# Kernel tuning notes

Hardware: AMD Instinct MI355X
Metric: run time of the kernel (lower is better)

## Reference

```python
import jax, jax.numpy as jnp
import numpy as np

INPUT_SIZE = 128
HIDDEN_SIZE = 128
BATCH = 65536
K = INPUT_SIZE + HIDDEN_SIZE


def setup_inputs() -> dict:
    key = jax.random.key(0)
    ks = jax.random.split(key, 11)
    bound = 1.0 / np.sqrt(K)  # nn.Linear default init range
    inp = {
        "input": jax.random.normal(ks[0], (BATCH, INPUT_SIZE), dtype=jnp.float32),
        "hidden": jax.random.normal(ks[1], (BATCH, HIDDEN_SIZE), dtype=jnp.float32),
        "cell": jax.random.normal(ks[2], (BATCH, HIDDEN_SIZE), dtype=jnp.float32),
        # Four gate linears: weights [hidden, K], biases [hidden]
        "W_f": jax.random.uniform(ks[3], (HIDDEN_SIZE, K), jnp.float32, -bound, bound),
        "b_f": jax.random.uniform(ks[4], (HIDDEN_SIZE,), jnp.float32, -bound, bound),
        "W_i": jax.random.uniform(ks[5], (HIDDEN_SIZE, K), jnp.float32, -bound, bound),
        "b_i": jax.random.uniform(ks[6], (HIDDEN_SIZE,), jnp.float32, -bound, bound),
        "W_o": jax.random.uniform(ks[7], (HIDDEN_SIZE, K), jnp.float32, -bound, bound),
        "b_o": jax.random.uniform(ks[8], (HIDDEN_SIZE,), jnp.float32, -bound, bound),
        "W_c": jax.random.uniform(ks[9], (HIDDEN_SIZE, K), jnp.float32, -bound, bound),
        "b_c": jax.random.uniform(ks[10], (HIDDEN_SIZE,), jnp.float32, -bound, bound),
    }
    return inp


def reference(input, hidden, cell, W_f, b_f, W_i, b_i, W_o, b_o, W_c, b_c):
    # combined = cat([input, hidden], axis=1); fuse 4 gate GEMMs into one
    combined = jnp.concatenate([input, hidden], axis=1)  # [B, K]
    W = jnp.concatenate([W_f, W_i, W_o, W_c], axis=0)    # [4H, K]
    b = jnp.concatenate([b_f, b_i, b_o, b_c], axis=0)    # [4H]
    gates = combined @ W.T + b                            # [B, 4H]
    f, i, o, g = jnp.split(gates, 4, axis=1)
    forget_gate = jax.nn.sigmoid(f)
    input_gate = jax.nn.sigmoid(i)
    output_gate = jax.nn.sigmoid(o)
    cell_gate = jnp.tanh(g)
    new_cell = forget_gate * cell + input_gate * cell_gate
    new_hidden = output_gate * jnp.tanh(new_cell)
    return (new_hidden, new_cell)
```

## Files before the change

kernel.cpp:

```cpp
#include <hip/hip_runtime.h>
#include <hip/hip_bf16.h>

#define BATCH   65536
#define FEAT    128
#define KDIM    256

typedef __attribute__((ext_vector_type(8))) short bf16x8;
typedef __attribute__((ext_vector_type(4))) float f32x4;

__device__ __forceinline__ short f2bf(float f) {
    return __builtin_bit_cast(short, __float2bfloat16(f));
}

__device__ __forceinline__ bf16x8 cvt8(f32x4 lo, f32x4 hi) {
    bf16x8 r;
    r[0] = f2bf(lo[0]); r[1] = f2bf(lo[1]); r[2] = f2bf(lo[2]); r[3] = f2bf(lo[3]);
    r[4] = f2bf(hi[0]); r[5] = f2bf(hi[1]); r[6] = f2bf(hi[2]); r[7] = f2bf(hi[3]);
    return r;
}

__device__ __forceinline__ float sigmoidf_(float x) {
    return 1.0f / (1.0f + __expf(-x));
}
__device__ __forceinline__ float tanhf_(float x) {
    float xc = fminf(fmaxf(x, -15.0f), 15.0f);
    float e = __expf(-2.0f * xc);
    return (1.0f - e) / (1.0f + e);
}

__global__ __launch_bounds__(256, 2)
void lstm_fused(const float* __restrict__ inp, const float* __restrict__ hid,
                const float* __restrict__ cel,
                const float* __restrict__ Wf, const float* __restrict__ bf_,
                const float* __restrict__ Wi, const float* __restrict__ bi_,
                const float* __restrict__ Wo, const float* __restrict__ bo_,
                const float* __restrict__ Wc, const float* __restrict__ bc_,
                float* __restrict__ out)
{
    const int tid  = threadIdx.x;
    const int lane = tid & 63;
    const int wid  = tid >> 6;
    const int b    = blockIdx.x;
    const int u      = b >> 3;
    const int xcd    = b & 7;
    const int rtBase = xcd * 32 + (u >> 1);
    const int cg     = ((u & 1) << 2) | wid;

    const int lr = lane & 15;
    const int lk = lane >> 4;
    const int j  = cg * 16 + lr;

    bf16x8 w[4][8];
    {
        const float* wsrc[4] = {Wf, Wi, Wo, Wc};
        #pragma unroll
        for (int g = 0; g < 4; ++g) {
            const float* src = wsrc[g] + (size_t)j * KDIM + lk * 8;
            #pragma unroll
            for (int ks = 0; ks < 8; ++ks) {
                f32x4 lo = *(const f32x4*)(src + ks * 32);
                f32x4 hi = *(const f32x4*)(src + ks * 32 + 4);
                w[g][ks] = cvt8(lo, hi);
            }
        }
    }
    const float bsf = bf_[j], bsi = bi_[j], bso = bo_[j], bsc = bc_[j];

    float* outH = out;
    float* outC = out + (size_t)BATCH * FEAT;

    for (int it = 0; it < 8; ++it) {
        const int R0 = (rtBase + it * 256) * 32;

        const float* aInp = inp + (size_t)(R0 + lr) * FEAT + lk * 8;
        const float* aHid = hid + (size_t)(R0 + lr) * FEAT + lk * 8;

        float cv[8];
        #pragma unroll
        for (int mb = 0; mb < 2; ++mb)
            #pragma unroll
            for (int t = 0; t < 4; ++t)
                cv[mb * 4 + t] = cel[(size_t)(R0 + mb * 16 + lk * 4 + t) * FEAT + j];

        f32x4 acc[2][4];
        #pragma unroll
        for (int mb = 0; mb < 2; ++mb)
            #pragma unroll
            for (int t = 0; t < 4; ++t) {
                acc[mb][0][t] = bsf; acc[mb][1][t] = bsi;
                acc[mb][2][t] = bso; acc[mb][3][t] = bsc;
            }

        f32x4 plo[2][2], phi[2][2];
        #pragma unroll
        for (int mb = 0; mb < 2; ++mb) {
            plo[0][mb] = *(const f32x4*)(aInp + mb * 16 * FEAT);
            phi[0][mb] = *(const f32x4*)(aInp + mb * 16 * FEAT + 4);
        }

        #pragma unroll
        for (int ks = 0; ks < 8; ++ks) {
            const int cur = ks & 1, nxt = cur ^ 1;
            if (ks < 7) {
                const float* nb2 = ((ks + 1) < 4 ? aInp : aHid) + ((ks + 1) & 3) * 32;
                #pragma unroll
                for (int mb = 0; mb < 2; ++mb) {
                    plo[nxt][mb] = *(const f32x4*)(nb2 + mb * 16 * FEAT);
                    phi[nxt][mb] = *(const f32x4*)(nb2 + mb * 16 * FEAT + 4);
                }
            }
            bf16x8 a0 = cvt8(plo[cur][0], phi[cur][0]);
            bf16x8 a1 = cvt8(plo[cur][1], phi[cur][1]);
            #pragma unroll
            for (int g = 0; g < 4; ++g) {
                acc[0][g] = __builtin_amdgcn_mfma_f32_16x16x32_bf16(a0, w[g][ks], acc[0][g], 0, 0, 0);
                acc[1][g] = __builtin_amdgcn_mfma_f32_16x16x32_bf16(a1, w[g][ks], acc[1][g], 0, 0, 0);
            }
        }

        #pragma unroll
        for (int mb = 0; mb < 2; ++mb) {
            #pragma unroll
            for (int t = 0; t < 4; ++t) {
                const int R = R0 + mb * 16 + lk * 4 + t;
                float fg = sigmoidf_(acc[mb][0][t]);
                float ig = sigmoidf_(acc[mb][1][t]);
                float og = sigmoidf_(acc[mb][2][t]);
                float gg = tanhf_(acc[mb][3][t]);
                float nc = fg * cv[mb * 4 + t] + ig * gg;
                float nh = og * tanhf_(nc);
                outH[(size_t)R * FEAT + j] = nh;
                outC[(size_t)R * FEAT + j] = nc;
            }
        }
    }
}

extern "C" void kernel_launch(void* const* d_in, const int* in_sizes, int n_in,
                              void* d_out, int out_size, void* d_ws, size_t ws_size,
                              hipStream_t stream) {
    const float* inp = (const float*)d_in[0];
    const float* hid = (const float*)d_in[1];
    const float* cel = (const float*)d_in[2];
    const float* Wf  = (const float*)d_in[3];
    const float* bf  = (const float*)d_in[4];
    const float* Wi  = (const float*)d_in[5];
    const float* bi  = (const float*)d_in[6];
    const float* Wo  = (const float*)d_in[7];
    const float* bo  = (const float*)d_in[8];
    const float* Wc  = (const float*)d_in[9];
    const float* bc  = (const float*)d_in[10];
    float* out = (float*)d_out;

    lstm_fused<<<dim3(512), dim3(256), 0, stream>>>(
        inp, hid, cel, Wf, bf, Wi, bi, Wo, bo, Wc, bc, out);
}
```

Before: 264.1 us.

## Split K across waves with LDS reduction in fused LSTM kernel

Each wave in a block now handles one quarter of the K dimension for a shared 16-column group instead of separate column groups. Partial gate accumulators go through shared memory and are reduced, then bias and the gate nonlinearities are applied. This cuts per-wave weight registers, which allows higher occupancy (launch bounds 4) and a grid of 1024 blocks. In exchange it adds LDS traffic, two block barriers per iteration, and drops the software prefetch of activations and the XCD-aware block mapping.

```diff
diff --git a/kernel.cpp b/kernel.cpp
--- a/kernel.cpp
+++ b/kernel.cpp
@@ -28,89 +28,75 @@
     return (1.0f - e) / (1.0f + e);
 }
 
-__global__ __launch_bounds__(256, 2)
-void lstm_fused(const float* __restrict__ inp, const float* __restrict__ hid,
-                const float* __restrict__ cel,
-                const float* __restrict__ Wf, const float* __restrict__ bf_,
-                const float* __restrict__ Wi, const float* __restrict__ bi_,
-                const float* __restrict__ Wo, const float* __restrict__ bo_,
-                const float* __restrict__ Wc, const float* __restrict__ bc_,
-                float* __restrict__ out)
+__global__ __launch_bounds__(256, 4)
+void lstm_ksplit(const float* __restrict__ inp, const float* __restrict__ hid,
+                 const float* __restrict__ cel,
+                 const float* __restrict__ Wf, const float* __restrict__ bfp,
+                 const float* __restrict__ Wi, const float* __restrict__ bip,
+                 const float* __restrict__ Wo, const float* __restrict__ bop,
+                 const float* __restrict__ Wc, const float* __restrict__ bcp,
+                 float* __restrict__ out)
 {
+    __shared__ float lds[4][64][35];
+
     const int tid  = threadIdx.x;
     const int lane = tid & 63;
     const int wid  = tid >> 6;
-    const int b    = blockIdx.x;
-    const int u      = b >> 3;
-    const int xcd    = b & 7;
-    const int rtBase = xcd * 32 + (u >> 1);
-    const int cg     = ((u & 1) << 2) | wid;
+    const int bid  = blockIdx.x;
+    const int cg   = bid >> 7;
+    const int rtg  = bid & 127;
 
     const int lr = lane & 15;
     const int lk = lane >> 4;
     const int j  = cg * 16 + lr;
 
-    bf16x8 w[4][8];
+    const int kq = wid;
+    const int k0 = (kq & 1) * 64;
+    const float* Asrc = (kq < 2) ? inp : hid;
+
+    bf16x8 w[4][2];
     {
         const float* wsrc[4] = {Wf, Wi, Wo, Wc};
         #pragma unroll
         for (int g = 0; g < 4; ++g) {
-            const float* src = wsrc[g] + (size_t)j * KDIM + lk * 8;
+            const float* s = wsrc[g] + (size_t)j * KDIM + kq * 64 + lk * 8;
             #pragma unroll
-            for (int ks = 0; ks < 8; ++ks) {
-                f32x4 lo = *(const f32x4*)(src + ks * 32);
-                f32x4 hi = *(const f32x4*)(src + ks * 32 + 4);
+            for (int ks = 0; ks < 2; ++ks) {
+                f32x4 lo = *(const f32x4*)(s + ks * 32);
+                f32x4 hi = *(const f32x4*)(s + ks * 32 + 4);
                 w[g][ks] = cvt8(lo, hi);
             }
         }
     }
-    const float bsf = bf_[j], bsi = bi_[j], bso = bo_[j], bsc = bc_[j];
+    const float bsf = bfp[j], bsi = bip[j], bso = bop[j], bsc = bcp[j];
 
     float* outH = out;
     float* outC = out + (size_t)BATCH * FEAT;
 
-    for (int it = 0; it < 8; ++it) {
-        const int R0 = (rtBase + it * 256) * 32;
+    for (int it = 0; it < 16; ++it) {
+        const int R0 = (rtg + it * 128) * 32;
 
-        const float* aInp = inp + (size_t)(R0 + lr) * FEAT + lk * 8;
-        const float* aHid = hid + (size_t)(R0 + lr) * FEAT + lk * 8;
-
-        float cv[8];
+        const float* a = Asrc + (size_t)(R0 + lr) * FEAT + k0 + lk * 8;
+        f32x4 alo[2][2], ahi[2][2];
         #pragma unroll
-        for (int mb = 0; mb < 2; ++mb)
+        for (int ks = 0; ks < 2; ++ks)
             #pragma unroll
-            for (int t = 0; t < 4; ++t)
-                cv[mb * 4 + t] = cel[(size_t)(R0 + mb * 16 + lk * 4 + t) * FEAT + j];
+            for (int mb = 0; mb < 2; ++mb) {
+                alo[ks][mb] = *(const f32x4*)(a + mb * 16 * FEAT + ks * 32);
+                ahi[ks][mb] = *(const f32x4*)(a + mb * 16 * FEAT + ks * 32 + 4);
+            }
 
         f32x4 acc[2][4];
         #pragma unroll
         for (int mb = 0; mb < 2; ++mb)
             #pragma unroll
-            for (int t = 0; t < 4; ++t) {
-                acc[mb][0][t] = bsf; acc[mb][1][t] = bsi;
-                acc[mb][2][t] = bso; acc[mb][3][t] = bsc;
-            }
-
-        f32x4 plo[2][2], phi[2][2];
-        #pragma unroll
-        for (int mb = 0; mb < 2; ++mb) {
-            plo[0][mb] = *(const f32x4*)(aInp + mb * 16 * FEAT);
-            phi[0][mb] = *(const f32x4*)(aInp + mb * 16 * FEAT + 4);
-        }
+            for (int g = 0; g < 4; ++g)
+                acc[mb][g] = (f32x4){0.f, 0.f, 0.f, 0.f};
 
         #pragma unroll
-        for (int ks = 0; ks < 8; ++ks) {
-            const int cur = ks & 1, nxt = cur ^ 1;
-            if (ks < 7) {
-                const float* nb2 = ((ks + 1) < 4 ? aInp : aHid) + ((ks + 1) & 3) * 32;
-                #pragma unroll
-                for (int mb = 0; mb < 2; ++mb) {
-                    plo[nxt][mb] = *(const f32x4*)(nb2 + mb * 16 * FEAT);
-                    phi[nxt][mb] = *(const f32x4*)(nb2 + mb * 16 * FEAT + 4);
-                }
-            }
-            bf16x8 a0 = cvt8(plo[cur][0], phi[cur][0]);
-            bf16x8 a1 = cvt8(plo[cur][1], phi[cur][1]);
+        for (int ks = 0; ks < 2; ++ks) {
+            bf16x8 a0 = cvt8(alo[ks][0], ahi[ks][0]);
+            bf16x8 a1 = cvt8(alo[ks][1], ahi[ks][1]);
             #pragma unroll
             for (int g = 0; g < 4; ++g) {
                 acc[0][g] = __builtin_amdgcn_mfma_f32_16x16x32_bf16(a0, w[g][ks], acc[0][g], 0, 0, 0);
@@ -119,20 +105,45 @@
         }
 
         #pragma unroll
-        for (int mb = 0; mb < 2; ++mb) {
+        for (int mb = 0; mb < 2; ++mb)
             #pragma unroll
-            for (int t = 0; t < 4; ++t) {
-                const int R = R0 + mb * 16 + lk * 4 + t;
-                float fg = sigmoidf_(acc[mb][0][t]);
-                float ig = sigmoidf_(acc[mb][1][t]);
-                float og = sigmoidf_(acc[mb][2][t]);
-                float gg = tanhf_(acc[mb][3][t]);
-                float nc = fg * cv[mb * 4 + t] + ig * gg;
-                float nh = og * tanhf_(nc);
-                outH[(size_t)R * FEAT + j] = nh;
-                outC[(size_t)R * FEAT + j] = nc;
+            for (int g = 0; g < 4; ++g)
+                #pragma unroll
+                for (int t = 0; t < 4; ++t)
+                    lds[kq][lane][mb * 16 + g * 4 + t] = acc[mb][g][t];
+        __syncthreads();
+
+        #pragma unroll
+        for (int p = 0; p < 2; ++p) {
+            const int rl  = wid * 8 + p * 4 + (lane >> 4);
+            const int jc  = lane & 15;
+            const int mb  = rl >> 4;
+            const int lk2 = (rl >> 2) & 3;
+            const int t   = rl & 3;
+            const int sl  = lk2 * 16 + jc;
+
+            float s0 = 0.f, s1 = 0.f, s2 = 0.f, s3 = 0.f;
+            #pragma unroll
+            for (int q = 0; q < 4; ++q) {
+                s0 += lds[q][sl][mb * 16 + 0 * 4 + t];
+                s1 += lds[q][sl][mb * 16 + 1 * 4 + t];
+                s2 += lds[q][sl][mb * 16 + 2 * 4 + t];
+                s3 += lds[q][sl][mb * 16 + 3 * 4 + t];
             }
+
+            const int R = R0 + rl;
+            const size_t off = (size_t)R * FEAT + cg * 16 + jc;
+            float cv = cel[off];
+            float fg = sigmoidf_(s0 + bsf);
+            float ig = sigmoidf_(s1 + bsi);
+            float og = sigmoidf_(s2 + bso);
+            float gg = tanhf_(s3 + bsc);
+            float nc = fg * cv + ig * gg;
+            float nh = og * tanhf_(nc);
+            outH[off] = nh;
+            outC[off] = nc;
         }
+        __syncthreads();
     }
 }
 
@@ -152,6 +163,6 @@
     const float* bc  = (const float*)d_in[10];
     float* out = (float*)d_out;
 
-    lstm_fused<<<dim3(512), dim3(256), 0, stream>>>(
+    lstm_ksplit<<<dim3(1024), dim3(256), 0, stream>>>(
         inp, hid, cel, Wf, bf, Wi, bi, Wo, bo, Wc, bc, out);
 }
```

Result: faster. 213.5 us (-19.2%).

## Pre-pack bf16 weights in a prep kernel and stream fragments from cache

Applied to the files above, without the earlier changes.

A separate prep kernel converts the four gate weight matrices to bf16 once, in MFMA fragment order, and writes them to workspace. The main kernel then uses 512-thread blocks covering all 128 columns per row tile, with 8 waves. It reloads weight fragments from global/L2 each iteration instead of holding them in registers, and prefetches wider activation chunks (64 K per step) across iterations. This removes the weight register footprint and the redundant per-block fp32-to-bf16 weight conversion. In exchange it adds a second launch and per-iteration weight loads that rely on cache hits.

```diff
diff --git a/kernel.cpp b/kernel.cpp
--- a/kernel.cpp
+++ b/kernel.cpp
@@ -28,52 +28,62 @@
     return (1.0f - e) / (1.0f + e);
 }
 
-__global__ __launch_bounds__(256, 2)
-void lstm_fused(const float* __restrict__ inp, const float* __restrict__ hid,
-                const float* __restrict__ cel,
-                const float* __restrict__ Wf, const float* __restrict__ bf_,
-                const float* __restrict__ Wi, const float* __restrict__ bi_,
-                const float* __restrict__ Wo, const float* __restrict__ bo_,
-                const float* __restrict__ Wc, const float* __restrict__ bc_,
-                float* __restrict__ out)
+__global__ __launch_bounds__(256)
+void prep_w(const float* __restrict__ Wf, const float* __restrict__ Wi,
+            const float* __restrict__ Wo, const float* __restrict__ Wc,
+            bf16x8* __restrict__ wsf)
+{
+    const int f    = blockIdx.x * 256 + threadIdx.x;
+    const int lane = f & 63;
+    const int ks   = (f >> 6) & 7;
+    const int g    = (f >> 9) & 3;
+    const int cg   = f >> 11;
+    const int lr   = lane & 15, lk = lane >> 4;
+    const float* W = (g == 0) ? Wf : (g == 1) ? Wi : (g == 2) ? Wo : Wc;
+    const float* s = W + (size_t)(cg * 16 + lr) * KDIM + ks * 32 + lk * 8;
+    wsf[f] = cvt8(*(const f32x4*)s, *(const f32x4*)(s + 4));
+}
+
+__global__ __launch_bounds__(512, 2)
+void lstm_v6(const float* __restrict__ inp, const float* __restrict__ hid,
+             const float* __restrict__ cel,
+             const float* __restrict__ bfp, const float* __restrict__ bip,
+             const float* __restrict__ bop, const float* __restrict__ bcp,
+             const bf16x8* __restrict__ wsf, float* __restrict__ out)
 {
     const int tid  = threadIdx.x;
     const int lane = tid & 63;
     const int wid  = tid >> 6;
-    const int b    = blockIdx.x;
-    const int u      = b >> 3;
-    const int xcd    = b & 7;
-    const int rtBase = xcd * 32 + (u >> 1);
-    const int cg     = ((u & 1) << 2) | wid;
+    const int bid  = blockIdx.x;
+    const int lr   = lane & 15;
+    const int lk   = lane >> 4;
+    const int j    = wid * 16 + lr;
 
-    const int lr = lane & 15;
-    const int lk = lane >> 4;
-    const int j  = cg * 16 + lr;
-
-    bf16x8 w[4][8];
-    {
-        const float* wsrc[4] = {Wf, Wi, Wo, Wc};
-        #pragma unroll
-        for (int g = 0; g < 4; ++g) {
-            const float* src = wsrc[g] + (size_t)j * KDIM + lk * 8;
-            #pragma unroll
-            for (int ks = 0; ks < 8; ++ks) {
-                f32x4 lo = *(const f32x4*)(src + ks * 32);
-                f32x4 hi = *(const f32x4*)(src + ks * 32 + 4);
-                w[g][ks] = cvt8(lo, hi);
-            }
-        }
-    }
-    const float bsf = bf_[j], bsi = bi_[j], bso = bo_[j], bsc = bc_[j];
+    const bf16x8* wfb0 = wsf + wid * 2048;
+    const float bsf = bfp[j], bsi = bip[j], bso = bop[j], bsc = bcp[j];
 
     float* outH = out;
     float* outC = out + (size_t)BATCH * FEAT;
 
-    for (int it = 0; it < 8; ++it) {
-        const int R0 = (rtBase + it * 256) * 32;
+    f32x4 slo[4], shi[4];
 
-        const float* aInp = inp + (size_t)(R0 + lr) * FEAT + lk * 8;
-        const float* aHid = hid + (size_t)(R0 + lr) * FEAT + lk * 8;
+    {
+        const float* a = inp + (size_t)(bid * 32 + lr) * FEAT + lk * 8;
+        #pragma unroll
+        for (int mb = 0; mb < 2; ++mb)
+            #pragma unroll
+            for (int c = 0; c < 2; ++c) {
+                slo[mb * 2 + c] = *(const f32x4*)(a + mb * 16 * FEAT + c * 32);
+                shi[mb * 2 + c] = *(const f32x4*)(a + mb * 16 * FEAT + c * 32 + 4);
+            }
+    }
+
+    for (int it = 0; it < 4; ++it) {
+        const int R0 = (bid + it * 512) * 32;
+
+        unsigned zoff = 0;
+        asm volatile("" : "+s"(zoff));
+        const bf16x8* wfb = wfb0 + zoff;
 
         float cv[8];
         #pragma unroll
@@ -84,55 +94,61 @@
 
         f32x4 acc[2][4];
         #pragma unroll
-        for (int mb = 0; mb < 2; ++mb)
-            #pragma unroll
-            for (int t = 0; t < 4; ++t) {
-                acc[mb][0][t] = bsf; acc[mb][1][t] = bsi;
-                acc[mb][2][t] = bso; acc[mb][3][t] = bsc;
-            }
-
-        f32x4 plo[2][2], phi[2][2];
-        #pragma unroll
         for (int mb = 0; mb < 2; ++mb) {
-            plo[0][mb] = *(const f32x4*)(aInp + mb * 16 * FEAT);
-            phi[0][mb] = *(const f32x4*)(aInp + mb * 16 * FEAT + 4);
+            acc[mb][0] = (f32x4){bsf, bsf, bsf, bsf};
+            acc[mb][1] = (f32x4){bsi, bsi, bsi, bsi};
+            acc[mb][2] = (f32x4){bso, bso, bso, bso};
+            acc[mb][3] = (f32x4){bsc, bsc, bsc, bsc};
         }
 
         #pragma unroll
-        for (int ks = 0; ks < 8; ++ks) {
-            const int cur = ks & 1, nxt = cur ^ 1;
-            if (ks < 7) {
-                const float* nb2 = ((ks + 1) < 4 ? aInp : aHid) + ((ks + 1) & 3) * 32;
+        for (int kq = 0; kq < 4; ++kq) {
+            bf16x8 afr[4];
+            #pragma unroll
+            for (int i = 0; i < 4; ++i) afr[i] = cvt8(slo[i], shi[i]);
+
+            if (it < 3 || kq < 3) {
+                const int kqn  = (kq + 1) & 3;
+                const int R0n  = (kq == 3) ? R0 + 512 * 32 : R0;
+                const float* S = (kqn < 2) ? inp : hid;
+                const float* a = S + (size_t)(R0n + lr) * FEAT + (kqn & 1) * 64 + lk * 8;
                 #pragma unroll
-                for (int mb = 0; mb < 2; ++mb) {
-                    plo[nxt][mb] = *(const f32x4*)(nb2 + mb * 16 * FEAT);
-                    phi[nxt][mb] = *(const f32x4*)(nb2 + mb * 16 * FEAT + 4);
+                for (int mb = 0; mb < 2; ++mb)
+                    #pragma unroll
+                    for (int c = 0; c < 2; ++c) {
+                        slo[mb * 2 + c] = *(const f32x4*)(a + mb * 16 * FEAT + c * 32);
+                        shi[mb * 2 + c] = *(const f32x4*)(a + mb * 16 * FEAT + c * 32 + 4);
+                    }
+            }
+
+            #pragma unroll
+            for (int c = 0; c < 2; ++c) {
+                const int ks = kq * 2 + c;
+                #pragma unroll
+                for (int g = 0; g < 4; ++g) {
+                    const bf16x8 wf = wfb[(g * 8 + ks) * 64 + lane];
+                    acc[0][g] = __builtin_amdgcn_mfma_f32_16x16x32_bf16(
+                        afr[0 * 2 + c], wf, acc[0][g], 0, 0, 0);
+                    acc[1][g] = __builtin_amdgcn_mfma_f32_16x16x32_bf16(
+                        afr[1 * 2 + c], wf, acc[1][g], 0, 0, 0);
                 }
-            }
-            bf16x8 a0 = cvt8(plo[cur][0], phi[cur][0]);
-            bf16x8 a1 = cvt8(plo[cur][1], phi[cur][1]);
-            #pragma unroll
-            for (int g = 0; g < 4; ++g) {
-                acc[0][g] = __builtin_amdgcn_mfma_f32_16x16x32_bf16(a0, w[g][ks], acc[0][g], 0, 0, 0);
-                acc[1][g] = __builtin_amdgcn_mfma_f32_16x16x32_bf16(a1, w[g][ks], acc[1][g], 0, 0, 0);
             }
         }
 
         #pragma unroll
-        for (int mb = 0; mb < 2; ++mb) {
+        for (int mb = 0; mb < 2; ++mb)
             #pragma unroll
             for (int t = 0; t < 4; ++t) {
-                const int R = R0 + mb * 16 + lk * 4 + t;
+                const size_t off = (size_t)(R0 + mb * 16 + lk * 4 + t) * FEAT + j;
                 float fg = sigmoidf_(acc[mb][0][t]);
                 float ig = sigmoidf_(acc[mb][1][t]);
                 float og = sigmoidf_(acc[mb][2][t]);
                 float gg = tanhf_(acc[mb][3][t]);
                 float nc = fg * cv[mb * 4 + t] + ig * gg;
                 float nh = og * tanhf_(nc);
-                outH[(size_t)R * FEAT + j] = nh;
-                outC[(size_t)R * FEAT + j] = nc;
+                outH[off] = nh;
+                outC[off] = nc;
             }
-        }
     }
 }
 
@@ -152,6 +168,9 @@
     const float* bc  = (const float*)d_in[10];
     float* out = (float*)d_out;
 
-    lstm_fused<<<dim3(512), dim3(256), 0, stream>>>(
-        inp, hid, cel, Wf, bf, Wi, bi, Wo, bo, Wc, bc, out);
+    bf16x8* wsf = (bf16x8*)d_ws;
+
+    prep_w<<<dim3(64), dim3(256), 0, stream>>>(Wf, Wi, Wo, Wc, wsf);
+    lstm_v6<<<dim3(512), dim3(512), 0, stream>>>(
+        inp, hid, cel, bf, bi, bo, bc, wsf, out);
 }
```

Measured after the change: 229.2 us. 13.2% less time.
